# Optimization experiments

Measured on AMD Instinct MI355X. Metric: run time of the kernel, lower is better.

The kernel has to match this reference:

```python
import jax, jax.numpy as jnp
import numpy as np

N_NODES = 100000
N_GRAPHS = 64


def gcn_layer(x, src, dst, W, b, n):
    # GCNConv: h = x @ W; out_i = sum_j norm_ij * h_j (+ self loop), + bias
    h = x @ W
    deg = jax.ops.segment_sum(jnp.ones(src.shape[0], x.dtype), dst, num_segments=n)
    dinv = jnp.where(deg > 0, jax.lax.rsqrt(deg), 0.0)
    norm = dinv[src] * dinv[dst]                      # [E+N]
    agg = jax.ops.segment_sum(h[src] * norm[:, None], dst, num_segments=n)
    return agg + b


def setup_inputs() -> dict:
    key = jax.random.key(0)
    ks = jax.random.split(key, 12)
    nfeat, nhid, nclass = 128, 64, 10
    E = 1600000
    x = jax.random.normal(ks[0], (N_NODES, nfeat), dtype=jnp.float32)
    edge_index = jax.random.randint(ks[1], (2, E), 0, N_NODES, dtype=jnp.int64)
    batch = jnp.sort(jax.random.randint(ks[2], (N_NODES,), 0, N_GRAPHS, dtype=jnp.int64))
    def w(k, fi, fo):
        return jax.random.normal(k, (fi, fo), dtype=jnp.float32) / np.sqrt(fi)
    return {
        "x": x, "edge_index": edge_index, "batch": batch,
        "W1": w(ks[3], nfeat, nhid), "b1": jnp.zeros((nhid,), jnp.float32),
        "W2": w(ks[4], nhid, nhid), "b2": jnp.zeros((nhid,), jnp.float32),
        "W3": w(ks[5], nhid, nhid), "b3": jnp.zeros((nhid,), jnp.float32),
        "Wl": w(ks[6], nhid, nclass), "bl": jnp.zeros((nclass,), jnp.float32),
    }


def reference(x, edge_index, batch, W1, b1, W2, b2, W3, b3, Wl, bl):
    n = x.shape[0]
    loop = jnp.arange(n, dtype=edge_index.dtype)
    src = jnp.concatenate([edge_index[0], loop])   # self-loops appended
    dst = jnp.concatenate([edge_index[1], loop])
    h = x  # eval mode: dropout is identity; use_bn=False
    for W, b in ((W1, b1), (W2, b2), (W3, b3)):
        h = jax.nn.relu(gcn_layer(h, src, dst, W, b, n))
    # global mean pool per graph
    sums = jax.ops.segment_sum(h, batch, num_segments=N_GRAPHS)
    cnts = jax.ops.segment_sum(jnp.ones((n,), h.dtype), batch, num_segments=N_GRAPHS)
    pooled = sums / jnp.maximum(cnts, 1.0)[:, None]   # [G, nhid]
    logits = pooled @ Wl + bl
    return jax.nn.softmax(logits, axis=1)
```

## Files before the change

### kernel.cpp

```cpp
#include <hip/hip_runtime.h>
#include <math.h>


typedef __attribute__((ext_vector_type(8))) short bf16x8;
typedef __attribute__((ext_vector_type(4))) float f32x4;

__device__ __forceinline__ unsigned short f2bf(float f) {
    unsigned int u = __float_as_uint(f);
    u += 0x7fffu + ((u >> 16) & 1u);
    return (unsigned short)(u >> 16);
}
__device__ __forceinline__ float bf2f(unsigned short u) {
    return __uint_as_float((unsigned int)u << 16);
}
__device__ __forceinline__ float bflo(unsigned int u) {
    return __uint_as_float(u << 16);
}
__device__ __forceinline__ float bfhi(unsigned int u) {
    return __uint_as_float(u & 0xffff0000u);
}


__global__ __launch_bounds__(256) void hist_kernel(const int* __restrict__ dst,
                                                   int* __restrict__ counts,
                                                   int E, int P, int C,
                                                   const float* __restrict__ W1,
                                                   const float* __restrict__ W2,
                                                   const float* __restrict__ W3,
                                                   unsigned short* __restrict__ Wt1,
                                                   unsigned short* __restrict__ Wt2,
                                                   unsigned short* __restrict__ Wt3,
                                                   float* __restrict__ sums, int G) {
    int t = threadIdx.x, b = blockIdx.x;
    if (b >= 256) {
        int xb = b - 256;
        if (xb < 3) {
            const float* W = (xb == 0) ? W1 : ((xb == 1) ? W2 : W3);
            unsigned short* Wt = (xb == 0) ? Wt1 : ((xb == 1) ? Wt2 : Wt3);
            int K = (xb == 0) ? 128 : 64;
            int o = t & 63;
            for (int k = t >> 6; k < K; k += 4)
                Wt[o * K + k] = f2bf(W[k * 64 + o]);
        } else {
            for (int i = t; i < G * 65; i += 256) sums[i] = 0.f;
        }
        return;
    }
    __shared__ int hist[256];
    if (t < P) hist[t] = 0;
    __syncthreads();
    int beg = b * C, end = min(E, beg + C);
    for (int e = beg + t; e < end; e += 256)
        atomicAdd(&hist[dst[e] >> 9], 1);
    __syncthreads();
    if (t < P) counts[t * 256 + b] = hist[t];
}

__global__ __launch_bounds__(256) void pscan_kernel(const int* __restrict__ counts,
                                                    int* __restrict__ pbase,
                                                    int P) {
    __shared__ int s[256];
    int t = threadIdx.x;
    int v = 0;
    if (t < P)
        for (int b = 0; b < 256; ++b) v += counts[t * 256 + b];
    s[t] = v;
    __syncthreads();
    for (int off = 1; off < 256; off <<= 1) {
        int u = (t >= off) ? s[t - off] : 0;
        __syncthreads();
        s[t] += u;
        __syncthreads();
    }
    if (t < P) pbase[t] = s[t] - v;
    if (t == 255) pbase[P] = s[255];
}

__global__ __launch_bounds__(256) void offs_kernel(const int* __restrict__ counts,
                                                   const int* __restrict__ pbase,
                                                   int* __restrict__ offs) {
    __shared__ int s[256];
    int t = threadIdx.x, p = blockIdx.x;
    int v = counts[p * 256 + t];
    s[t] = v;
    __syncthreads();
    for (int off = 1; off < 256; off <<= 1) {
        int u = (t >= off) ? s[t - off] : 0;
        __syncthreads();
        s[t] += u;
        __syncthreads();
    }
    offs[p * 256 + t] = pbase[p] + s[t] - v;
}

__global__ __launch_bounds__(256) void bin_kernel(const int* __restrict__ src,
                                                  const int* __restrict__ dst,
                                                  const int* __restrict__ offs,
                                                  unsigned int* __restrict__ binned,
                                                  int E, int P, int C) {
    __shared__ int cur[256];
    int t = threadIdx.x, b = blockIdx.x;
    if (t < P) cur[t] = offs[t * 256 + b];
    __syncthreads();
    int beg = b * C, end = min(E, beg + C);
    for (int e = beg + t; e < end; e += 256) {
        int d = dst[e], s = src[e];
        int pos = atomicAdd(&cur[d >> 9], 1);
        binned[pos] = ((unsigned int)s << 9) | (unsigned int)(d & 511);
    }
}

__global__ __launch_bounds__(512) void lsortA_kernel(const unsigned int* __restrict__ binned,
                                                     const int* __restrict__ pbase,
                                                     int* __restrict__ rowptr,
                                                     float* __restrict__ dinv,
                                                     int* __restrict__ partTot8, int N) {
    __shared__ int ldeg[512];
    __shared__ int s[512];
    int t = threadIdx.x, p = blockIdx.x;
    int lo = p << 9;
    ldeg[t] = 0;
    __syncthreads();
    int eBeg = pbase[p], eEnd = pbase[p + 1];
    for (int j = eBeg + t; j < eEnd; j += 512)
        atomicAdd(&ldeg[binned[j] & 511u], 1);
    __syncthreads();
    int real = ldeg[t];
    int a = (lo + t < N) ? ((real + 1 + 7) & ~7) : 0;
    s[t] = a;
    __syncthreads();
    for (int off = 1; off < 512; off <<= 1) {
        int u = (t >= off) ? s[t - off] : 0;
        __syncthreads();
        s[t] += u;
        __syncthreads();
    }
    if (lo + t < N) {
        rowptr[lo + t] = s[t] - a;
        dinv[lo + t] = rsqrtf((float)(real + 1));
    }
    if (t == 511) partTot8[p] = s[511];
}

__global__ __launch_bounds__(256) void pscan8_kernel(const int* __restrict__ partTot8,
                                                     int* __restrict__ pbase8,
                                                     int* __restrict__ rowptr,
                                                     int P, int N) {
    __shared__ int s[256];
    int t = threadIdx.x;
    int v = (t < P) ? partTot8[t] : 0;
    s[t] = v;
    __syncthreads();
    for (int off = 1; off < 256; off <<= 1) {
        int u = (t >= off) ? s[t - off] : 0;
        __syncthreads();
        s[t] += u;
        __syncthreads();
    }
    if (t < P) pbase8[t] = s[t] - v;
    if (t == 255) { pbase8[P] = s[255]; rowptr[N] = s[255]; }
}

__global__ __launch_bounds__(256) void lsortB_kernel(const unsigned int* __restrict__ binned,
                                                     const int* __restrict__ pbase,
                                                     const int* __restrict__ pbase8,
                                                     int* __restrict__ rowptr,
                                                     const float* __restrict__ dinv,
                                                     float2* __restrict__ csrw, int N) {
    __shared__ int srow[513];
    __shared__ int cur[512];
    __shared__ float sdi[512];
    int t = threadIdx.x, p = blockIdx.x;
    int lo = p << 9, span = min(N - lo, 512);
    int b8 = pbase8[p];
    for (int i = t; i < span; i += 256) {
        int r = rowptr[lo + i] + b8;
        srow[i] = r;
        cur[i] = r;
        sdi[i] = dinv[lo + i];
        rowptr[lo + i] = r;
    }
    if (t == 0) srow[span] = pbase8[p + 1];
    __syncthreads();
    int eBeg = pbase[p], eEnd = pbase[p + 1];
    for (int j = eBeg + t; j < eEnd; j += 256) {
        unsigned int v = binned[j];
        int s = (int)(v >> 9);
        int dl = (int)(v & 511u);
        int pos = atomicAdd(&cur[dl], 1);
        csrw[pos] = make_float2(__int_as_float(s << 7), dinv[s] * sdi[dl]);
    }
    __syncthreads();
    for (int i = t; i < span; i += 256) {
        int c = cur[i];
        float d = sdi[i];
        csrw[c] = make_float2(__int_as_float((lo + i) << 7), d * d);
        int nxt = srow[i + 1];
        for (int k = c + 1; k < nxt; ++k)
            csrw[k] = make_float2(0.f, 0.f);
    }
}

template <int FIN, bool F32IN>
__global__ __launch_bounds__(256) void gemm_mfma_kernel(const void* __restrict__ Xv,
                                                        const unsigned short* __restrict__ Wt,
                                                        unsigned short* __restrict__ H,
                                                        int N) {
    constexpr int KS = FIN / 32;
    int wave = threadIdx.x >> 6;
    int lane = threadIdx.x & 63;
    int r = lane & 15, g = lane >> 4;
    int node = blockIdx.x * 64 + wave * 16 + r;
    int nodeL = min(node, N - 1);

    bf16x8 afr[4][KS];
#pragma unroll
    for (int m = 0; m < 4; ++m)
#pragma unroll
        for (int s = 0; s < KS; ++s)
            afr[m][s] = *(const bf16x8*)&Wt[(m * 16 + r) * FIN + s * 32 + g * 8];

    f32x4 acc[4];
#pragma unroll
    for (int m = 0; m < 4; ++m) acc[m] = (f32x4){0.f, 0.f, 0.f, 0.f};

#pragma unroll
    for (int s = 0; s < KS; ++s) {
        bf16x8 bfr;
        if (F32IN) {
            const float* X = (const float*)Xv + (size_t)nodeL * FIN + s * 32 + g * 8;
            float4 lo = *(const float4*)X;
            float4 hi = *(const float4*)(X + 4);
            unsigned e0 = __float_as_uint(lo.x) + 0x8000u, e1 = __float_as_uint(lo.y) + 0x8000u;
            unsigned e2 = __float_as_uint(lo.z) + 0x8000u, e3 = __float_as_uint(lo.w) + 0x8000u;
            unsigned e4 = __float_as_uint(hi.x) + 0x8000u, e5 = __float_as_uint(hi.y) + 0x8000u;
            unsigned e6 = __float_as_uint(hi.z) + 0x8000u, e7 = __float_as_uint(hi.w) + 0x8000u;
            int4 rv;
            rv.x = __builtin_amdgcn_perm(e1, e0, 0x07060302);
            rv.y = __builtin_amdgcn_perm(e3, e2, 0x07060302);
            rv.z = __builtin_amdgcn_perm(e5, e4, 0x07060302);
            rv.w = __builtin_amdgcn_perm(e7, e6, 0x07060302);
            bfr = *(bf16x8*)&rv;
        } else {
            bfr = *(const bf16x8*)((const unsigned short*)Xv + (size_t)nodeL * FIN + s * 32 + g * 8);
        }
#pragma unroll
        for (int m = 0; m < 4; ++m)
            acc[m] = __builtin_amdgcn_mfma_f32_16x16x32_bf16(afr[m][s], bfr, acc[m], 0, 0, 0);
    }

    if (node < N) {
#pragma unroll
        for (int m = 0; m < 4; ++m) {
            ushort4 o;
            o.x = f2bf(acc[m][0]); o.y = f2bf(acc[m][1]);
            o.z = f2bf(acc[m][2]); o.w = f2bf(acc[m][3]);
            *(ushort4*)&H[(size_t)node * 64 + m * 16 + g * 4] = o;
        }
    }
}

template <int NQ>
__device__ __forceinline__ void gstep(const float2* __restrict__ csrw,
                                      const char* __restrict__ hb,
                                      int e, int g, int fo, float acc[8]) {
    float2 c[NQ];
#pragma unroll
    for (int q = 0; q < NQ; ++q) c[q] = csrw[e + 8 * q + g];
    uint4 u[NQ];
#pragma unroll
    for (int q = 0; q < NQ; ++q)
        u[q] = *(const uint4*)(hb + __float_as_int(c[q].x) + fo);
#pragma unroll
    for (int q = 0; q < NQ; ++q) {
        float wq = c[q].y;
        acc[0] = fmaf(wq, bflo(u[q].x), acc[0]);
        acc[1] = fmaf(wq, bfhi(u[q].x), acc[1]);
        acc[2] = fmaf(wq, bflo(u[q].y), acc[2]);
        acc[3] = fmaf(wq, bfhi(u[q].y), acc[3]);
        acc[4] = fmaf(wq, bflo(u[q].z), acc[4]);
        acc[5] = fmaf(wq, bfhi(u[q].z), acc[5]);
        acc[6] = fmaf(wq, bflo(u[q].w), acc[6]);
        acc[7] = fmaf(wq, bfhi(u[q].w), acc[7]);
    }
}

__global__ __launch_bounds__(256) void gather_kernel(const float2* __restrict__ csrw,
                                                     const int* __restrict__ rowptr,
                                                     const unsigned short* __restrict__ h,
                                                     const float* __restrict__ b,
                                                     unsigned short* __restrict__ aggb, int N) {
    int node = (blockIdx.x * 256 + threadIdx.x) >> 6;
    int lane = threadIdx.x & 63;
    if (node >= N) return;
    int g = lane >> 3;
    int f = lane & 7;
    int fo = f * 16;
    int beg = rowptr[node], end = rowptr[node + 1];

    float acc[8];
#pragma unroll
    for (int k = 0; k < 8; ++k) acc[k] = 0.f;

    const char* hb = (const char*)h;
    int e = beg;
    while (e + 32 <= end) { gstep<4>(csrw, hb, e, g, fo, acc); e += 32; }
    if (e + 16 <= end)    { gstep<2>(csrw, hb, e, g, fo, acc); e += 16; }
    if (e + 8 <= end)     { gstep<1>(csrw, hb, e, g, fo, acc); }

#pragma unroll
    for (int k = 0; k < 8; ++k) {
        float v = acc[k];
        v += __shfl_xor(v, 8);
        v += __shfl_xor(v, 16);
        v += __shfl_xor(v, 32);
        acc[k] = v;
    }
    if (g == 0) {
        float4 bv0 = *(const float4*)&b[f * 8];
        float4 bv1 = *(const float4*)&b[f * 8 + 4];
        float a0 = fmaxf(acc[0] + bv0.x, 0.f), a1 = fmaxf(acc[1] + bv0.y, 0.f);
        float a2 = fmaxf(acc[2] + bv0.z, 0.f), a3 = fmaxf(acc[3] + bv0.w, 0.f);
        float a4 = fmaxf(acc[4] + bv1.x, 0.f), a5 = fmaxf(acc[5] + bv1.y, 0.f);
        float a6 = fmaxf(acc[6] + bv1.z, 0.f), a7 = fmaxf(acc[7] + bv1.w, 0.f);
        uint4 o;
        o.x = ((unsigned)f2bf(a1) << 16) | f2bf(a0);
        o.y = ((unsigned)f2bf(a3) << 16) | f2bf(a2);
        o.z = ((unsigned)f2bf(a5) << 16) | f2bf(a4);
        o.w = ((unsigned)f2bf(a7) << 16) | f2bf(a6);
        *(uint4*)&aggb[((size_t)node << 6) + f * 8] = o;
    }
}

__global__ __launch_bounds__(256) void pool_kernel(const unsigned short* __restrict__ hb,
                                                   const int* __restrict__ batch,
                                                   float* __restrict__ sums,
                                                   float* __restrict__ cnts, int N) {
    int col = threadIdx.x & 63;
    int wave = threadIdx.x >> 6;
    int base = blockIdx.x * 256 + wave * 64;
    float acc = 0.f, cnt = 0.f;
    int curg = -1;
    for (int j = 0; j < 64; ++j) {
        int node = base + j;
        if (node >= N) break;
        int g = batch[node];
        if (g != curg) {
            if (curg >= 0) {
                atomicAdd(&sums[curg * 64 + col], acc);
                if (col == 0) atomicAdd(&cnts[curg], cnt);
            }
            acc = 0.f; cnt = 0.f;
            curg = g;
        }
        acc += bf2f(hb[(size_t)node * 64 + col]);
        cnt += 1.f;
    }
    if (curg >= 0) {
        atomicAdd(&sums[curg * 64 + col], acc);
        if (col == 0) atomicAdd(&cnts[curg], cnt);
    }
}

__global__ void final_kernel(const float* __restrict__ sums, const float* __restrict__ cnts,
                             const float* __restrict__ Wl, const float* __restrict__ bl,
                             float* __restrict__ out, int G) {
    int g = blockIdx.x * blockDim.x + threadIdx.x;
    if (g >= G) return;
    float inv = 1.0f / fmaxf(cnts[g], 1.0f);
    float logits[10];
#pragma unroll
    for (int k = 0; k < 10; ++k) logits[k] = bl[k];
    for (int c = 0; c < 64; ++c) {
        float p = sums[g * 64 + c] * inv;
#pragma unroll
        for (int k = 0; k < 10; ++k) logits[k] = fmaf(p, Wl[c * 10 + k], logits[k]);
    }
    float m = logits[0];
#pragma unroll
    for (int k = 1; k < 10; ++k) m = fmaxf(m, logits[k]);
    float se = 0.f;
#pragma unroll
    for (int k = 0; k < 10; ++k) { logits[k] = expf(logits[k] - m); se += logits[k]; }
    float is = 1.0f / se;
#pragma unroll
    for (int k = 0; k < 10; ++k) out[g * 10 + k] = logits[k] * is;
}

extern "C" void kernel_launch(void* const* d_in, const int* in_sizes, int n_in,
                              void* d_out, int out_size, void* d_ws, size_t ws_size,
                              hipStream_t stream) {
    const float* x    = (const float*)d_in[0];
    const int* edges  = (const int*)d_in[1];
    const int* batch  = (const int*)d_in[2];
    const float* W1   = (const float*)d_in[3];
    const float* b1   = (const float*)d_in[4];
    const float* W2   = (const float*)d_in[5];
    const float* b2   = (const float*)d_in[6];
    const float* W3   = (const float*)d_in[7];
    const float* b3   = (const float*)d_in[8];
    const float* Wl   = (const float*)d_in[9];
    const float* bl   = (const float*)d_in[10];

    const int N = in_sizes[0] / 128;
    const int E = in_sizes[1] / 2;
    const int G = out_size / 10;
    const int* src = edges;
    const int* dst = edges + E;

    float* ws     = (float*)d_ws;
    unsigned short* h = (unsigned short*)ws;
    unsigned short* aggb = (unsigned short*)(ws + (size_t)N * 64);
    unsigned int* binned = (unsigned int*)ws;
    size_t csrwOff = (size_t)2 * N * 64;
    float2* csrw  = (float2*)(ws + csrwOff);
    size_t o = csrwOff + (size_t)2 * (E + 8 * N);
    float* dinv   = ws + o;            o += N;
    int*   rowptr = (int*)(ws + o);    o += N + 1;
    int*   counts = (int*)(ws + o);    o += 256 * 256;
    int*   offs   = (int*)(ws + o);    o += 256 * 256;
    int*   pbase  = (int*)(ws + o);    o += 257;
    float* sums   = ws + o;            o += (size_t)G * 64;
    float* cnts   = ws + o;            o += G;
    int*   partTot8 = (int*)(ws + o);  o += 256;
    int*   pbase8 = (int*)(ws + o);    o += 257;
    unsigned short* Wt1 = (unsigned short*)(ws + o);
    unsigned short* Wt2 = Wt1 + 64 * 128;
    unsigned short* Wt3 = Wt2 + 64 * 64;

    const int gemmGrid = (N + 63) / 64;
    const int gatherGrid = (N + 3) / 4;
    const int P = (N + 511) >> 9;
    const int C = (E + 255) / 256;

    hist_kernel<<<260, 256, 0, stream>>>(dst, counts, E, P, C,
                                         W1, W2, W3, Wt1, Wt2, Wt3, sums, G);
    pscan_kernel<<<1, 256, 0, stream>>>(counts, pbase, P);
    offs_kernel<<<P, 256, 0, stream>>>(counts, pbase, offs);
    bin_kernel<<<256, 256, 0, stream>>>(src, dst, offs, binned, E, P, C);
    lsortA_kernel<<<P, 512, 0, stream>>>(binned, pbase, rowptr, dinv, partTot8, N);
    pscan8_kernel<<<1, 256, 0, stream>>>(partTot8, pbase8, rowptr, P, N);
    lsortB_kernel<<<P, 256, 0, stream>>>(binned, pbase, pbase8, rowptr, dinv, csrw, N);

    gemm_mfma_kernel<128, true><<<gemmGrid, 256, 0, stream>>>(x, Wt1, h, N);
    gather_kernel<<<gatherGrid, 256, 0, stream>>>(csrw, rowptr, h, b1, aggb, N);

    gemm_mfma_kernel<64, false><<<gemmGrid, 256, 0, stream>>>(aggb, Wt2, h, N);
    gather_kernel<<<gatherGrid, 256, 0, stream>>>(csrw, rowptr, h, b2, aggb, N);

    gemm_mfma_kernel<64, false><<<gemmGrid, 256, 0, stream>>>(aggb, Wt3, h, N);
    gather_kernel<<<gatherGrid, 256, 0, stream>>>(csrw, rowptr, h, b3, aggb, N);

    pool_kernel<<<(N + 255) / 256, 256, 0, stream>>>(aggb, batch, sums, cnts, N);
    final_kernel<<<1, 64, 0, stream>>>(sums, cnts, Wl, bl, (float*)d_out, G);
}
```

Baseline: 387.3 us.

## Fuse partition scan into lsortB, stage GEMM inputs in LDS, batch pool loads

Drops the separate pscan8 launch: every lsortB block now recomputes the prefix scan of partition totals itself. The GEMM kernel first loads each 64-row input tile into padded shared memory with coalesced vector loads, so the MFMA loop no longer issues strided global loads per lane. The pool kernel assigns 32 nodes per wave, loads all values up front and reads batch ids by shuffle rather than serial per-node loads. The cost is redundant scan work in each lsortB block, extra LDS and a barrier in the GEMM, and higher register use in pool.

```diff
diff --git a/kernel.cpp b/kernel.cpp
--- a/kernel.cpp
+++ b/kernel.cpp
@@ -142,37 +142,30 @@
     if (t == 511) partTot8[p] = s[511];
 }
 
-__global__ __launch_bounds__(256) void pscan8_kernel(const int* __restrict__ partTot8,
-                                                     int* __restrict__ pbase8,
-                                                     int* __restrict__ rowptr,
-                                                     int P, int N) {
-    __shared__ int s[256];
-    int t = threadIdx.x;
-    int v = (t < P) ? partTot8[t] : 0;
-    s[t] = v;
-    __syncthreads();
-    for (int off = 1; off < 256; off <<= 1) {
-        int u = (t >= off) ? s[t - off] : 0;
-        __syncthreads();
-        s[t] += u;
-        __syncthreads();
-    }
-    if (t < P) pbase8[t] = s[t] - v;
-    if (t == 255) { pbase8[P] = s[255]; rowptr[N] = s[255]; }
-}
-
 __global__ __launch_bounds__(256) void lsortB_kernel(const unsigned int* __restrict__ binned,
                                                      const int* __restrict__ pbase,
-                                                     const int* __restrict__ pbase8,
+                                                     const int* __restrict__ partTot8,
                                                      int* __restrict__ rowptr,
                                                      const float* __restrict__ dinv,
-                                                     float2* __restrict__ csrw, int N) {
+                                                     float2* __restrict__ csrw, int N, int P) {
+    __shared__ int s[256];
     __shared__ int srow[513];
     __shared__ int cur[512];
     __shared__ float sdi[512];
     int t = threadIdx.x, p = blockIdx.x;
+    int v = (t < P) ? partTot8[t] : 0;
+    s[t] = v;
+    __syncthreads();
+    for (int off = 1; off < 256; off <<= 1) {
+        int u = (t >= off) ? s[t - off] : 0;
+        __syncthreads();
+        s[t] += u;
+        __syncthreads();
+    }
+    int b8 = s[p] - partTot8[p];
+    int endP = s[p];
+    if (p == 0 && t == 0) rowptr[N] = s[P - 1];
     int lo = p << 9, span = min(N - lo, 512);
-    int b8 = pbase8[p];
     for (int i = t; i < span; i += 256) {
         int r = rowptr[lo + i] + b8;
         srow[i] = r;
@@ -180,15 +173,15 @@
         sdi[i] = dinv[lo + i];
         rowptr[lo + i] = r;
     }
-    if (t == 0) srow[span] = pbase8[p + 1];
+    if (t == 0) srow[span] = endP;
     __syncthreads();
     int eBeg = pbase[p], eEnd = pbase[p + 1];
     for (int j = eBeg + t; j < eEnd; j += 256) {
-        unsigned int v = binned[j];
-        int s = (int)(v >> 9);
-        int dl = (int)(v & 511u);
+        unsigned int vv = binned[j];
+        int sr = (int)(vv >> 9);
+        int dl = (int)(vv & 511u);
         int pos = atomicAdd(&cur[dl], 1);
-        csrw[pos] = make_float2(__int_as_float(s << 7), dinv[s] * sdi[dl]);
+        csrw[pos] = make_float2(__int_as_float(sr << 7), dinv[sr] * sdi[dl]);
     }
     __syncthreads();
     for (int i = t; i < span; i += 256) {
@@ -207,11 +200,37 @@
                                                         unsigned short* __restrict__ H,
                                                         int N) {
     constexpr int KS = FIN / 32;
-    int wave = threadIdx.x >> 6;
-    int lane = threadIdx.x & 63;
+    constexpr int LDP = FIN + 8;
+    __shared__ unsigned short sX[64 * LDP];
+    int tid = threadIdx.x;
+    int rowBase = blockIdx.x * 64;
+
+    if (F32IN) {
+        for (int i = tid * 4; i < 64 * FIN; i += 1024) {
+            int r = i / FIN, c = i - r * FIN;
+            int gr = min(rowBase + r, N - 1);
+            float4 vv = *(const float4*)((const float*)Xv + (size_t)gr * FIN + c);
+            unsigned e0 = __float_as_uint(vv.x) + 0x8000u, e1 = __float_as_uint(vv.y) + 0x8000u;
+            unsigned e2 = __float_as_uint(vv.z) + 0x8000u, e3 = __float_as_uint(vv.w) + 0x8000u;
+            uint2 pk;
+            pk.x = __builtin_amdgcn_perm(e1, e0, 0x07060302);
+            pk.y = __builtin_amdgcn_perm(e3, e2, 0x07060302);
+            *(uint2*)&sX[r * LDP + c] = pk;
+        }
+    } else {
+        for (int i = tid * 8; i < 64 * FIN; i += 2048) {
+            int r = i / FIN, c = i - r * FIN;
+            int gr = min(rowBase + r, N - 1);
+            uint4 vv = *(const uint4*)((const unsigned short*)Xv + (size_t)gr * FIN + c);
+            *(uint4*)&sX[r * LDP + c] = vv;
+        }
+    }
+    __syncthreads();
+
+    int wave = tid >> 6;
+    int lane = tid & 63;
     int r = lane & 15, g = lane >> 4;
-    int node = blockIdx.x * 64 + wave * 16 + r;
-    int nodeL = min(node, N - 1);
+    int node = rowBase + wave * 16 + r;
 
     bf16x8 afr[4][KS];
 #pragma unroll
@@ -226,24 +245,7 @@
 
 #pragma unroll
     for (int s = 0; s < KS; ++s) {
-        bf16x8 bfr;
-        if (F32IN) {
-            const float* X = (const float*)Xv + (size_t)nodeL * FIN + s * 32 + g * 8;
-            float4 lo = *(const float4*)X;
-            float4 hi = *(const float4*)(X + 4);
-            unsigned e0 = __float_as_uint(lo.x) + 0x8000u, e1 = __float_as_uint(lo.y) + 0x8000u;
-            unsigned e2 = __float_as_uint(lo.z) + 0x8000u, e3 = __float_as_uint(lo.w) + 0x8000u;
-            unsigned e4 = __float_as_uint(hi.x) + 0x8000u, e5 = __float_as_uint(hi.y) + 0x8000u;
-            unsigned e6 = __float_as_uint(hi.z) + 0x8000u, e7 = __float_as_uint(hi.w) + 0x8000u;
-            int4 rv;
-            rv.x = __builtin_amdgcn_perm(e1, e0, 0x07060302);
-            rv.y = __builtin_amdgcn_perm(e3, e2, 0x07060302);
-            rv.z = __builtin_amdgcn_perm(e5, e4, 0x07060302);
-            rv.w = __builtin_amdgcn_perm(e7, e6, 0x07060302);
-            bfr = *(bf16x8*)&rv;
-        } else {
-            bfr = *(const bf16x8*)((const unsigned short*)Xv + (size_t)nodeL * FIN + s * 32 + g * 8);
-        }
+        bf16x8 bfr = *(const bf16x8*)&sX[(wave * 16 + r) * LDP + s * 32 + g * 8];
 #pragma unroll
         for (int m = 0; m < 4; ++m)
             acc[m] = __builtin_amdgcn_mfma_f32_16x16x32_bf16(afr[m][s], bfr, acc[m], 0, 0, 0);
@@ -336,30 +338,36 @@
                                                    const int* __restrict__ batch,
                                                    float* __restrict__ sums,
                                                    float* __restrict__ cnts, int N) {
-    int col = threadIdx.x & 63;
-    int wave = threadIdx.x >> 6;
-    int base = blockIdx.x * 256 + wave * 64;
+    int lane = threadIdx.x & 63;
+    int wid = (blockIdx.x * 256 + threadIdx.x) >> 6;
+    int base = wid * 32;
+    if (base >= N) return;
+    int nn = min(N - base, 32);
+    int bl = batch[base + min(lane & 31, nn - 1)];
+
+    float v[32];
+#pragma unroll
+    for (int j = 0; j < 32; ++j) {
+        int node = base + min(j, nn - 1);
+        v[j] = bf2f(hb[(size_t)node * 64 + lane]);
+    }
+
+    int curg = __shfl(bl, 0);
     float acc = 0.f, cnt = 0.f;
-    int curg = -1;
-    for (int j = 0; j < 64; ++j) {
-        int node = base + j;
-        if (node >= N) break;
-        int g = batch[node];
-        if (g != curg) {
-            if (curg >= 0) {
-                atomicAdd(&sums[curg * 64 + col], acc);
-                if (col == 0) atomicAdd(&cnts[curg], cnt);
+#pragma unroll
+    for (int j = 0; j < 32; ++j) {
+        if (j < nn) {
+            int g = __shfl(bl, j);
+            if (g != curg) {
+                atomicAdd(&sums[curg * 64 + lane], acc);
+                if (lane == 0) atomicAdd(&cnts[curg], cnt);
+                acc = 0.f; cnt = 0.f; curg = g;
             }
-            acc = 0.f; cnt = 0.f;
-            curg = g;
+            acc += v[j]; cnt += 1.f;
         }
-        acc += bf2f(hb[(size_t)node * 64 + col]);
-        cnt += 1.f;
-    }
-    if (curg >= 0) {
-        atomicAdd(&sums[curg * 64 + col], acc);
-        if (col == 0) atomicAdd(&cnts[curg], cnt);
-    }
+    }
+    atomicAdd(&sums[curg * 64 + lane], acc);
+    if (lane == 0) atomicAdd(&cnts[curg], cnt);
 }
 
 __global__ void final_kernel(const float* __restrict__ sums, const float* __restrict__ cnts,
@@ -423,13 +431,13 @@
     float* sums   = ws + o;            o += (size_t)G * 64;
     float* cnts   = ws + o;            o += G;
     int*   partTot8 = (int*)(ws + o);  o += 256;
-    int*   pbase8 = (int*)(ws + o);    o += 257;
     unsigned short* Wt1 = (unsigned short*)(ws + o);
     unsigned short* Wt2 = Wt1 + 64 * 128;
     unsigned short* Wt3 = Wt2 + 64 * 64;
 
     const int gemmGrid = (N + 63) / 64;
     const int gatherGrid = (N + 3) / 4;
+    const int poolGrid = ((N + 31) / 32 + 3) / 4;
     const int P = (N + 511) >> 9;
     const int C = (E + 255) / 256;
 
@@ -439,8 +447,7 @@
     offs_kernel<<<P, 256, 0, stream>>>(counts, pbase, offs);
     bin_kernel<<<256, 256, 0, stream>>>(src, dst, offs, binned, E, P, C);
     lsortA_kernel<<<P, 512, 0, stream>>>(binned, pbase, rowptr, dinv, partTot8, N);
-    pscan8_kernel<<<1, 256, 0, stream>>>(partTot8, pbase8, rowptr, P, N);
-    lsortB_kernel<<<P, 256, 0, stream>>>(binned, pbase, pbase8, rowptr, dinv, csrw, N);
+    lsortB_kernel<<<P, 256, 0, stream>>>(binned, pbase, partTot8, rowptr, dinv, csrw, N, P);
 
     gemm_mfma_kernel<128, true><<<gemmGrid, 256, 0, stream>>>(x, Wt1, h, N);
     gather_kernel<<<gatherGrid, 256, 0, stream>>>(csrw, rowptr, h, b1, aggb, N);
@@ -451,6 +458,6 @@
     gemm_mfma_kernel<64, false><<<gemmGrid, 256, 0, stream>>>(aggb, Wt3, h, N);
     gather_kernel<<<gatherGrid, 256, 0, stream>>>(csrw, rowptr, h, b3, aggb, N);
 
-    pool_kernel<<<(N + 255) / 256, 256, 0, stream>>>(aggb, batch, sums, cnts, N);
+    pool_kernel<<<poolGrid, 256, 0, stream>>>(aggb, batch, sums, cnts, N);
     final_kernel<<<1, 64, 0, stream>>>(sums, cnts, Wl, bl, (float*)d_out, G);
 }
```

Measured after the change: 367.5 us. 1.05x faster.
